# Optimization experiments

Measured on AMD Instinct MI355X. Metric: run time of the kernel, lower is better.

Reference implementation:

```python
import jax, jax.numpy as jnp
import numpy as np

D_MODEL = 1024
N_HEADS = 16
D_K = D_MODEL // N_HEADS
B, T = 2, 2048
EPS = 1e-6


def _phi(x):
    # elu(x) + 1
    return jax.nn.elu(x) + 1.0


def setup_inputs() -> dict:
    key = jax.random.key(0)
    ks = jax.random.split(key, 5)
    s = 1.0 / np.sqrt(D_MODEL)
    return {
        "x": jax.random.normal(ks[0], (B, T, D_MODEL), jnp.float32),
        "Wq": jax.random.normal(ks[1], (D_MODEL, D_MODEL), jnp.float32) * s,
        "bq": jnp.zeros((D_MODEL,), jnp.float32),
        "Wk": jax.random.normal(ks[2], (D_MODEL, D_MODEL), jnp.float32) * s,
        "bk": jnp.zeros((D_MODEL,), jnp.float32),
        "Wv": jax.random.normal(ks[3], (D_MODEL, D_MODEL), jnp.float32) * s,
        "bv": jnp.zeros((D_MODEL,), jnp.float32),
        "Wo": jax.random.normal(ks[4], (D_MODEL, D_MODEL), jnp.float32) * s,
        "bo": jnp.zeros((D_MODEL,), jnp.float32),
    }


def reference(x, Wq, bq, Wk, bk, Wv, bv, Wo, bo):
    Bv_, Tv_, _ = x.shape
    # projections (torch nn.Linear: x @ W.T + b), split heads -> [B, H, T, d_k]
    def proj(W, b):
        y = x @ W.T + b
        return y.reshape(Bv_, Tv_, N_HEADS, D_K).transpose(0, 2, 1, 3)

    q = _phi(proj(Wq, bq))
    k = _phi(proj(Wk, bk))
    v = proj(Wv, bv)

    # causal linear attention: running kv outer-product and k prefix sums
    kv = jnp.einsum("bhtd,bhte->bhtde", k, v)          # [B,H,T,d_k,d_k]
    kv = jnp.cumsum(kv, axis=2)
    k_cum = jnp.cumsum(k, axis=2)
    out = jnp.einsum("bhtd,bhtde->bhte", q, kv)        # [B,H,T,d_k]
    z = jnp.einsum("bhtd,bhtd->bht", q, k_cum)         # [B,H,T]
    out = out / (z[..., None] + EPS)

    out = out.transpose(0, 2, 1, 3).reshape(Bv_, Tv_, N_HEADS * D_K)
    return out @ Wo.T + bo
```

## Files before the change

### kernel.cpp

```cpp
#include <hip/hip_runtime.h>


typedef float  f32x4   __attribute__((ext_vector_type(4)));
typedef __bf16 bf16x8  __attribute__((ext_vector_type(8)));
typedef short  short8v __attribute__((ext_vector_type(8)));
typedef short  short4v __attribute__((ext_vector_type(4)));

static __device__ __forceinline__ short f2bf(float f) {
    unsigned u = __float_as_uint(f);
    u += 0x7FFFu + ((u >> 16) & 1u);
    return (short)(u >> 16);
}
static __device__ __forceinline__ float bf2f(short s) {
    return __uint_as_float(((unsigned)(unsigned short)s) << 16);
}
static __device__ __forceinline__ float phi(float x) {
    return x > 0.f ? x + 1.f : __expf(x);
}
static __device__ __forceinline__ void gl_lds16(const short* g, short* l) {
    __builtin_amdgcn_global_load_lds(
        (const __attribute__((address_space(1))) void*)g,
        (__attribute__((address_space(3))) void*)l, 16, 0, 0);
}

#define LDT 72
static __device__ __forceinline__ int swz(int row, int col) {
    return row * LDT + (col ^ (row & 56));
}

__global__ __launch_bounds__(256) void convert_bf16(
    const float* __restrict__ x,  const float* __restrict__ Wq,
    const float* __restrict__ Wk, const float* __restrict__ Wv,
    const float* __restrict__ Wo,
    short* __restrict__ xb,  short* __restrict__ Wqb,
    short* __restrict__ Wkb, short* __restrict__ Wvb, short* __restrict__ Wob)
{
    const int blk = blockIdx.x;
    const float* src; short* dst; size_t base;
    if (blk < 2048)      { src = x;  dst = xb;  base = (size_t)blk * 2048; }
    else if (blk < 2560) { src = Wq; dst = Wqb; base = (size_t)(blk - 2048) * 2048; }
    else if (blk < 3072) { src = Wk; dst = Wkb; base = (size_t)(blk - 2560) * 2048; }
    else if (blk < 3584) { src = Wv; dst = Wvb; base = (size_t)(blk - 3072) * 2048; }
    else                 { src = Wo; dst = Wob; base = (size_t)(blk - 3584) * 2048; }
    const size_t o = base + (size_t)threadIdx.x * 8;
    f32x4 v0 = *(const f32x4*)&src[o];
    f32x4 v1 = *(const f32x4*)&src[o + 4];
    short8v s;
#pragma unroll
    for (int m = 0; m < 4; ++m) { s[m] = f2bf(v0[m]); s[m + 4] = f2bf(v1[m]); }
    *(short8v*)&dst[o] = s;
}

__global__ __launch_bounds__(256) void gemm_qkv(
    const short* __restrict__ xb,
    const short* __restrict__ Wqb, const short* __restrict__ Wkb,
    const short* __restrict__ Wvb,
    const float* __restrict__ bq, const float* __restrict__ bk,
    const float* __restrict__ bv,
    short* __restrict__ Qb, short* __restrict__ Kb, short* __restrict__ Vb)
{
    __shared__ short As[128 * 32];
    __shared__ short Bs[128 * 32];
    const int tid = threadIdx.x;
    const int bm = blockIdx.x, bn = blockIdx.y;
    const int wsel = bn >> 3;
    const int n0 = (bn & 7) << 7;
    const short* __restrict__ W    = (wsel == 0) ? Wqb : (wsel == 1) ? Wkb : Wvb;
    const float* __restrict__ bias = (wsel == 0) ? bq  : (wsel == 1) ? bk  : bv;
    short* __restrict__ Ob         = (wsel == 0) ? Qb  : (wsel == 1) ? Kb  : Vb;
    const int m0 = bm << 7;
    const int wave = tid >> 6, lane = tid & 63;
    const int wm = (wave & 1) << 6, wn = (wave >> 1) << 6;
    const int l15 = lane & 15, quad = lane >> 4;

    const int ch0 = wave * 2, ch1 = ch0 + 1;
    const int lrow = lane >> 2, lcol = (lane & 3) << 3;
    const short* ga0 = xb + (size_t)(m0 + ch0 * 16 + lrow) * 1024 + lcol;
    const short* ga1 = xb + (size_t)(m0 + ch1 * 16 + lrow) * 1024 + lcol;
    const short* gb0 = W  + (size_t)(n0 + ch0 * 16 + lrow) * 1024 + lcol;
    const short* gb1 = W  + (size_t)(n0 + ch1 * 16 + lrow) * 1024 + lcol;
    short* la0 = &As[ch0 * 512];
    short* la1 = &As[ch1 * 512];
    short* lb0 = &Bs[ch0 * 512];
    short* lb1 = &Bs[ch1 * 512];

    f32x4 acc[4][4] = {};
    for (int k0 = 0; k0 < 1024; k0 += 32) {
        __syncthreads();
        gl_lds16(ga0 + k0, la0);
        gl_lds16(ga1 + k0, la1);
        gl_lds16(gb0 + k0, lb0);
        gl_lds16(gb1 + k0, lb1);
        __syncthreads();
        bf16x8 a[4], b[4];
#pragma unroll
        for (int i = 0; i < 4; ++i) a[i] = *(const bf16x8*)&As[(wm + i * 16 + l15) * 32 + quad * 8];
#pragma unroll
        for (int j = 0; j < 4; ++j) b[j] = *(const bf16x8*)&Bs[(wn + j * 16 + l15) * 32 + quad * 8];
#pragma unroll
        for (int i = 0; i < 4; ++i)
#pragma unroll
            for (int j = 0; j < 4; ++j)
                acc[i][j] = __builtin_amdgcn_mfma_f32_16x16x32_bf16(a[i], b[j], acc[i][j], 0, 0, 0);
    }

#pragma unroll
    for (int i = 0; i < 4; ++i)
#pragma unroll
        for (int j = 0; j < 4; ++j) {
            const int col = n0 + wn + j * 16 + l15;
            const int h = col >> 6, d = col & 63;
            const float bv_ = bias[col];
            const int row0 = m0 + wm + i * 16 + quad * 4;
            const int b = row0 >> 11, t0 = row0 & 2047;
            const size_t obase = ((size_t)(b * 16 + h) * 2048 + t0) * 64 + d;
#pragma unroll
            for (int r = 0; r < 4; ++r) {
                float v = acc[i][j][r] + bv_;
                if (wsel < 2) v = phi(v);
                Ob[obase + (size_t)r * 64] = f2bf(v);
            }
        }
}

__global__ __launch_bounds__(256) void chunk_sums(
    const short* __restrict__ Kb, const short* __restrict__ Vb,
    short* __restrict__ KVsum, float* __restrict__ ksum)
{
    __shared__ short KT[64 * LDT];
    __shared__ short VT[64 * LDT];
    __shared__ float pS[256];
    const int c = blockIdx.x, bh = blockIdx.y;
    const int tid = threadIdx.x;
    const int w = tid >> 6, lane = tid & 63, l15 = lane & 15, quad = lane >> 4;
    const size_t tilebase = ((size_t)bh * 2048 + c * 64) * 64;

    {
        const int t0 = (tid >> 4) << 2;
        const int e0 = (tid & 15) << 2;
        short4v kr[4], vr[4];
#pragma unroll
        for (int i = 0; i < 4; ++i) {
            const size_t g = tilebase + (size_t)(t0 + i) * 64 + e0;
            kr[i] = *(const short4v*)&Kb[g];
            vr[i] = *(const short4v*)&Vb[g];
        }
#pragma unroll
        for (int i = 0; i < 4; ++i) {
            short4v kt, vt;
#pragma unroll
            for (int j = 0; j < 4; ++j) { kt[j] = kr[j][i]; vt[j] = vr[j][i]; }
            *(short4v*)&KT[swz(e0 + i, t0)] = kt;
            *(short4v*)&VT[swz(e0 + i, t0)] = vt;
        }
    }
    __syncthreads();

    f32x4 acc[4] = {};
    __builtin_amdgcn_s_setprio(1);
#pragma unroll
    for (int k0 = 0; k0 < 64; k0 += 32) {
        const int ra = w * 16 + l15;
        bf16x8 a = *(const bf16x8*)&KT[ra * LDT + ((k0 + quad * 8) ^ (ra & 56))];
#pragma unroll
        for (int tj = 0; tj < 4; ++tj) {
            const int rb = tj * 16 + l15;
            bf16x8 bfr = *(const bf16x8*)&VT[rb * LDT + ((k0 + quad * 8) ^ (rb & 56))];
            acc[tj] = __builtin_amdgcn_mfma_f32_16x16x32_bf16(a, bfr, acc[tj], 0, 0, 0);
        }
    }
    __builtin_amdgcn_s_setprio(0);
    short* __restrict__ outp = KVsum + (((size_t)bh * 32) + c) * 4096;
#pragma unroll
    for (int tj = 0; tj < 4; ++tj)
#pragma unroll
        for (int r = 0; r < 4; ++r)
            outp[(w * 16 + quad * 4 + r) * 64 + tj * 16 + l15] = f2bf(acc[tj][r]);

    {
        const int d = tid & 63, part = tid >> 6;
        short8v k1 = *(const short8v*)&KT[d * LDT + ((part * 16) ^ (d & 56))];
        short8v k2 = *(const short8v*)&KT[d * LDT + ((part * 16 + 8) ^ (d & 56))];
        float s = 0.f;
#pragma unroll
        for (int m = 0; m < 8; ++m) s += bf2f(k1[m]) + bf2f(k2[m]);
        pS[part * 64 + d] = s;
    }
    __syncthreads();
    if (tid < 64)
        ksum[(((size_t)bh * 32) + c) * 64 + tid] =
            pS[tid] + pS[tid + 64] + pS[tid + 128] + pS[tid + 192];
}

__global__ __launch_bounds__(256) void scan_chunks(
    const short* __restrict__ KVsum, const float* __restrict__ ksum,
    short* __restrict__ KVpref, float* __restrict__ kpref)
{
    const int bh = blockIdx.y;
    const int o = blockIdx.x * 256 + threadIdx.x;
    float run = 0.f;
    size_t base = (size_t)bh * 32 * 4096 + o;
    for (int cc = 0; cc < 32; ++cc) {
        KVpref[base] = f2bf(run);
        run += bf2f(KVsum[base]);
        base += 4096;
    }
    if (blockIdx.x == 0 && threadIdx.x < 64) {
        float vals[32];
        const size_t kb = (size_t)bh * 32 * 64 + threadIdx.x;
#pragma unroll
        for (int cc = 0; cc < 32; ++cc) vals[cc] = ksum[kb + (size_t)cc * 64];
        float r2 = 0.f;
#pragma unroll
        for (int cc = 0; cc < 32; ++cc) { kpref[kb + (size_t)cc * 64] = r2; r2 += vals[cc]; }
    }
}

__global__ __launch_bounds__(256) void attn_chunk(
    const short* __restrict__ Qb, const short* __restrict__ Kb,
    const short* __restrict__ Vb, const short* __restrict__ KVpref,
    const float* __restrict__ kpref, short* __restrict__ attnb)
{
    __shared__ short Qs[64 * LDT];
    __shared__ short KS[64 * LDT];
    __shared__ short VT[64 * LDT];
    __shared__ short KVT[64 * LDT];
    const int c = blockIdx.x, bh = blockIdx.y;
    const int b = bh >> 4, h = bh & 15;
    const int tid = threadIdx.x;
    const int w = tid >> 6, lane = tid & 63, l15 = lane & 15, quad = lane >> 4;
    const size_t tilebase = ((size_t)bh * 2048 + c * 64) * 64;
    const short* __restrict__ KVc = KVpref + (((size_t)bh * 32) + c) * 4096;

#pragma unroll
    for (int p = 0; p < 2; ++p) {
        const int t = (tid >> 3) + p * 32;
        const int e0q = (tid & 7) << 3;
        const size_t g = tilebase + (size_t)t * 64 + e0q;
        *(short8v*)&Qs[t * LDT + e0q] = *(const short8v*)&Qb[g];
        *(short8v*)&KS[t * LDT + e0q] = *(const short8v*)&Kb[g];
    }
    {
        const int t0 = (tid >> 4) << 2;
        const int e0 = (tid & 15) << 2;
        short4v vr[4], pr[4];
#pragma unroll
        for (int i = 0; i < 4; ++i) {
            const size_t g = tilebase + (size_t)(t0 + i) * 64 + e0;
            vr[i] = *(const short4v*)&Vb[g];
            pr[i] = *(const short4v*)&KVc[(t0 + i) * 64 + e0];
        }
#pragma unroll
        for (int i = 0; i < 4; ++i) {
            short4v vt, pt;
#pragma unroll
            for (int j = 0; j < 4; ++j) { vt[j] = vr[j][i]; pt[j] = pr[j][i]; }
            *(short4v*)&VT[swz(e0 + i, t0)]  = vt;
            *(short4v*)&KVT[swz(e0 + i, t0)] = pt;
        }
    }
    __syncthreads();

    f32x4 sacc[4] = {};
    __builtin_amdgcn_s_setprio(1);
#pragma unroll
    for (int k0 = 0; k0 < 64; k0 += 32) {
        bf16x8 a = *(const bf16x8*)&Qs[(w * 16 + l15) * LDT + k0 + quad * 8];
#pragma unroll
        for (int tj = 0; tj < 4; ++tj) {
            bf16x8 bfr = *(const bf16x8*)&KS[(tj * 16 + l15) * LDT + k0 + quad * 8];
            sacc[tj] = __builtin_amdgcn_mfma_f32_16x16x32_bf16(a, bfr, sacc[tj], 0, 0, 0);
        }
    }
    __builtin_amdgcn_s_setprio(0);

    f32x4 kp4 = *(const f32x4*)&kpref[(((size_t)bh * 32) + c) * 64 + l15 * 4];
    float zinv[4];
#pragma unroll
    for (int r = 0; r < 4; ++r) {
        const int i = w * 16 + quad * 4 + r;
        float p = 0.f;
#pragma unroll
        for (int tj = 0; tj < 4; ++tj)
            if (tj * 16 + l15 <= i) p += sacc[tj][r];
        short4v q4 = *(const short4v*)&Qs[i * LDT + l15 * 4];
#pragma unroll
        for (int m = 0; m < 4; ++m) p += bf2f(q4[m]) * kp4[m];
        p += __shfl_xor(p, 1);
        p += __shfl_xor(p, 2);
        p += __shfl_xor(p, 4);
        p += __shfl_xor(p, 8);
        zinv[r] = 1.f / (p + 1e-6f);
    }

    __syncthreads();
#pragma unroll
    for (int tj = 0; tj < 4; ++tj)
#pragma unroll
        for (int r = 0; r < 4; ++r) {
            const int i = w * 16 + quad * 4 + r;
            const int j = tj * 16 + l15;
            KS[i * LDT + j] = f2bf(j <= i ? sacc[tj][r] : 0.f);
        }

    f32x4 oacc[4] = {};
    __builtin_amdgcn_s_setprio(1);
#pragma unroll
    for (int k0 = 0; k0 < 64; k0 += 32) {
        bf16x8 a1 = *(const bf16x8*)&KS[(w * 16 + l15) * LDT + k0 + quad * 8];
        bf16x8 a2 = *(const bf16x8*)&Qs[(w * 16 + l15) * LDT + k0 + quad * 8];
#pragma unroll
        for (int tj = 0; tj < 4; ++tj) {
            const int rb = tj * 16 + l15;
            bf16x8 b1 = *(const bf16x8*)&VT[rb * LDT + ((k0 + quad * 8) ^ (rb & 56))];
            bf16x8 b2 = *(const bf16x8*)&KVT[rb * LDT + ((k0 + quad * 8) ^ (rb & 56))];
            oacc[tj] = __builtin_amdgcn_mfma_f32_16x16x32_bf16(a1, b1, oacc[tj], 0, 0, 0);
            oacc[tj] = __builtin_amdgcn_mfma_f32_16x16x32_bf16(a2, b2, oacc[tj], 0, 0, 0);
        }
    }
    __builtin_amdgcn_s_setprio(0);
    const size_t arowbase = (size_t)b * 2048 + c * 64;
#pragma unroll
    for (int tj = 0; tj < 4; ++tj)
#pragma unroll
        for (int r = 0; r < 4; ++r) {
            const int i = w * 16 + quad * 4 + r;
            const int e = tj * 16 + l15;
            attnb[(arowbase + i) * 1024 + h * 64 + e] = f2bf(oacc[tj][r] * zinv[r]);
        }
}

__global__ __launch_bounds__(256) void gemm_out(
    const short* __restrict__ attnb, const short* __restrict__ Wob,
    const float* __restrict__ bo, float* __restrict__ outp)
{
    __shared__ short As[128 * 32];
    __shared__ short Bs[64 * 32];
    const int tid = threadIdx.x;
    const int bm = blockIdx.x, bn = blockIdx.y;
    const int m0 = bm << 7, n0 = bn << 6;
    const int wave = tid >> 6, lane = tid & 63;
    const int wm = (wave & 1) << 6, wn = (wave >> 1) << 5;
    const int l15 = lane & 15, quad = lane >> 4;

    const int lrow = lane >> 2, lcol = (lane & 3) << 3;
    const short* gp[3]; short* lp[3];
#pragma unroll
    for (int cc = 0; cc < 3; ++cc) {
        const int ch = wave * 3 + cc;
        if (ch < 8) {
            gp[cc] = attnb + (size_t)(m0 + ch * 16 + lrow) * 1024 + lcol;
            lp[cc] = &As[ch * 512];
        } else {
            gp[cc] = Wob + (size_t)(n0 + (ch - 8) * 16 + lrow) * 1024 + lcol;
            lp[cc] = &Bs[(ch - 8) * 512];
        }
    }

    f32x4 acc[4][2] = {};
    for (int k0 = 0; k0 < 1024; k0 += 32) {
        __syncthreads();
        gl_lds16(gp[0] + k0, lp[0]);
        gl_lds16(gp[1] + k0, lp[1]);
        gl_lds16(gp[2] + k0, lp[2]);
        __syncthreads();
        bf16x8 a[4], b[2];
#pragma unroll
        for (int i = 0; i < 4; ++i) a[i] = *(const bf16x8*)&As[(wm + i * 16 + l15) * 32 + quad * 8];
#pragma unroll
        for (int j = 0; j < 2; ++j) b[j] = *(const bf16x8*)&Bs[(wn + j * 16 + l15) * 32 + quad * 8];
#pragma unroll
        for (int i = 0; i < 4; ++i)
#pragma unroll
            for (int j = 0; j < 2; ++j)
                acc[i][j] = __builtin_amdgcn_mfma_f32_16x16x32_bf16(a[i], b[j], acc[i][j], 0, 0, 0);
    }

#pragma unroll
    for (int i = 0; i < 4; ++i)
#pragma unroll
        for (int j = 0; j < 2; ++j) {
            const int col = n0 + wn + j * 16 + l15;
            const float bv_ = bo[col];
#pragma unroll
            for (int r = 0; r < 4; ++r) {
                const int row = m0 + wm + i * 16 + quad * 4 + r;
                outp[(size_t)row * 1024 + col] = acc[i][j][r] + bv_;
            }
        }
}

extern "C" void kernel_launch(void* const* d_in, const int* in_sizes, int n_in,
                              void* d_out, int out_size, void* d_ws, size_t ws_size,
                              hipStream_t stream)
{
    const float* x  = (const float*)d_in[0];
    const float* Wq = (const float*)d_in[1];
    const float* bq = (const float*)d_in[2];
    const float* Wk = (const float*)d_in[3];
    const float* bk = (const float*)d_in[4];
    const float* Wv = (const float*)d_in[5];
    const float* bv = (const float*)d_in[6];
    const float* Wo = (const float*)d_in[7];
    const float* bo = (const float*)d_in[8];

    char* ws = (char*)d_ws;
    short* xb     = (short*)(ws + 0);
    short* Wqb    = (short*)(ws + 8388608);
    short* Wkb    = (short*)(ws + 10485760);
    short* Wvb    = (short*)(ws + 12582912);
    short* Wob    = (short*)(ws + 14680064);
    short* Qb     = (short*)(ws + 16777216);
    short* Kb     = (short*)(ws + 25165824);
    short* Vb     = (short*)(ws + 33554432);
    short* KVsum  = (short*)(ws + 41943040);
    short* KVpref = (short*)(ws + 50331648);
    short* attnb  = (short*)(ws + 58720256);
    float* ksum   = (float*)(ws + 67108864);
    float* kpref  = (float*)(ws + 67371008);
    float* outp   = (float*)d_out;

    convert_bf16<<<4096, 256, 0, stream>>>(x, Wq, Wk, Wv, Wo, xb, Wqb, Wkb, Wvb, Wob);
    gemm_qkv   <<<dim3(32, 24), 256, 0, stream>>>(xb, Wqb, Wkb, Wvb, bq, bk, bv, Qb, Kb, Vb);
    chunk_sums <<<dim3(32, 32), 256, 0, stream>>>(Kb, Vb, KVsum, ksum);
    scan_chunks<<<dim3(16, 32), 256, 0, stream>>>(KVsum, ksum, KVpref, kpref);
    attn_chunk <<<dim3(32, 32), 256, 0, stream>>>(Qb, Kb, Vb, KVpref, kpref, attnb);
    gemm_out   <<<dim3(32, 16), 256, 0, stream>>>(attnb, Wob, bo, outp);
}
```

Measured before the change: 161.6 us.

## Fuse chunk prefix scan into attention kernel, dropping scan_chunks launch

Removes the separate scan_chunks kernel. Each attn_chunk block now sums the KV chunk sums and k sums of all earlier chunks itself to build its prefix state. This saves one launch and the KVpref/kpref write and read round trip. In exchange, the work becomes redundant: block c reads c earlier 8KB tiles, giving O(C^2) total reads and an imbalanced load that grows with chunk index.

```diff
diff --git a/kernel.cpp b/kernel.cpp
--- a/kernel.cpp
+++ b/kernel.cpp
@@ -192,34 +192,10 @@
             pS[tid] + pS[tid + 64] + pS[tid + 128] + pS[tid + 192];
 }
 
-__global__ __launch_bounds__(256) void scan_chunks(
-    const short* __restrict__ KVsum, const float* __restrict__ ksum,
-    short* __restrict__ KVpref, float* __restrict__ kpref)
-{
-    const int bh = blockIdx.y;
-    const int o = blockIdx.x * 256 + threadIdx.x;
-    float run = 0.f;
-    size_t base = (size_t)bh * 32 * 4096 + o;
-    for (int cc = 0; cc < 32; ++cc) {
-        KVpref[base] = f2bf(run);
-        run += bf2f(KVsum[base]);
-        base += 4096;
-    }
-    if (blockIdx.x == 0 && threadIdx.x < 64) {
-        float vals[32];
-        const size_t kb = (size_t)bh * 32 * 64 + threadIdx.x;
-#pragma unroll
-        for (int cc = 0; cc < 32; ++cc) vals[cc] = ksum[kb + (size_t)cc * 64];
-        float r2 = 0.f;
-#pragma unroll
-        for (int cc = 0; cc < 32; ++cc) { kpref[kb + (size_t)cc * 64] = r2; r2 += vals[cc]; }
-    }
-}
-
 __global__ __launch_bounds__(256) void attn_chunk(
     const short* __restrict__ Qb, const short* __restrict__ Kb,
-    const short* __restrict__ Vb, const short* __restrict__ KVpref,
-    const float* __restrict__ kpref, short* __restrict__ attnb)
+    const short* __restrict__ Vb, const short* __restrict__ KVsum,
+    const float* __restrict__ ksum, short* __restrict__ attnb)
 {
     __shared__ short Qs[64 * LDT];
     __shared__ short KS[64 * LDT];
@@ -230,7 +206,7 @@
     const int tid = threadIdx.x;
     const int w = tid >> 6, lane = tid & 63, l15 = lane & 15, quad = lane >> 4;
     const size_t tilebase = ((size_t)bh * 2048 + c * 64) * 64;
-    const short* __restrict__ KVc = KVpref + (((size_t)bh * 32) + c) * 4096;
+    const short* __restrict__ KVbase = KVsum + ((size_t)bh * 32) * 4096;
 
 #pragma unroll
     for (int p = 0; p < 2; ++p) {
@@ -240,23 +216,45 @@
         *(short8v*)&Qs[t * LDT + e0q] = *(const short8v*)&Qb[g];
         *(short8v*)&KS[t * LDT + e0q] = *(const short8v*)&Kb[g];
     }
+    const int t0 = (tid >> 4) << 2;
+    const int e0 = (tid & 15) << 2;
     {
-        const int t0 = (tid >> 4) << 2;
-        const int e0 = (tid & 15) << 2;
-        short4v vr[4], pr[4];
+        short4v vr[4];
+#pragma unroll
+        for (int i = 0; i < 4; ++i)
+            vr[i] = *(const short4v*)&Vb[tilebase + (size_t)(t0 + i) * 64 + e0];
 #pragma unroll
         for (int i = 0; i < 4; ++i) {
-            const size_t g = tilebase + (size_t)(t0 + i) * 64 + e0;
-            vr[i] = *(const short4v*)&Vb[g];
-            pr[i] = *(const short4v*)&KVc[(t0 + i) * 64 + e0];
-        }
+            short4v vt;
+#pragma unroll
+            for (int j = 0; j < 4; ++j) vt[j] = vr[j][i];
+            *(short4v*)&VT[swz(e0 + i, t0)] = vt;
+        }
+    }
+    float pacc[4][4] = {};
+    for (int cc = 0; cc < c; ++cc) {
+        const short* tp = KVbase + (size_t)cc * 4096;
 #pragma unroll
         for (int i = 0; i < 4; ++i) {
-            short4v vt, pt;
-#pragma unroll
-            for (int j = 0; j < 4; ++j) { vt[j] = vr[j][i]; pt[j] = pr[j][i]; }
-            *(short4v*)&VT[swz(e0 + i, t0)]  = vt;
-            *(short4v*)&KVT[swz(e0 + i, t0)] = pt;
+            short4v s = *(const short4v*)&tp[(t0 + i) * 64 + e0];
+#pragma unroll
+            for (int j = 0; j < 4; ++j) pacc[i][j] += bf2f(s[j]);
+        }
+    }
+#pragma unroll
+    for (int j = 0; j < 4; ++j) {
+        short4v pt;
+#pragma unroll
+        for (int i = 0; i < 4; ++i) pt[i] = f2bf(pacc[i][j]);
+        *(short4v*)&KVT[swz(e0 + j, t0)] = pt;
+    }
+    f32x4 kp4 = {0.f, 0.f, 0.f, 0.f};
+    {
+        const float* kb_ = ksum + ((size_t)bh * 32) * 64 + l15 * 4;
+        for (int cc = 0; cc < c; ++cc) {
+            f32x4 kv = *(const f32x4*)&kb_[(size_t)cc * 64];
+#pragma unroll
+            for (int m = 0; m < 4; ++m) kp4[m] += kv[m];
         }
     }
     __syncthreads();
@@ -274,7 +272,6 @@
     }
     __builtin_amdgcn_s_setprio(0);
 
-    f32x4 kp4 = *(const f32x4*)&kpref[(((size_t)bh * 32) + c) * 64 + l15 * 4];
     float zinv[4];
 #pragma unroll
     for (int r = 0; r < 4; ++r) {
@@ -414,16 +411,13 @@
     short* Kb     = (short*)(ws + 25165824);
     short* Vb     = (short*)(ws + 33554432);
     short* KVsum  = (short*)(ws + 41943040);
-    short* KVpref = (short*)(ws + 50331648);
-    short* attnb  = (short*)(ws + 58720256);
-    float* ksum   = (float*)(ws + 67108864);
-    float* kpref  = (float*)(ws + 67371008);
+    short* attnb  = (short*)(ws + 50331648);
+    float* ksum   = (float*)(ws + 58720256);
     float* outp   = (float*)d_out;
 
     convert_bf16<<<4096, 256, 0, stream>>>(x, Wq, Wk, Wv, Wo, xb, Wqb, Wkb, Wvb, Wob);
     gemm_qkv   <<<dim3(32, 24), 256, 0, stream>>>(xb, Wqb, Wkb, Wvb, bq, bk, bv, Qb, Kb, Vb);
     chunk_sums <<<dim3(32, 32), 256, 0, stream>>>(Kb, Vb, KVsum, ksum);
-    scan_chunks<<<dim3(16, 32), 256, 0, stream>>>(KVsum, ksum, KVpref, kpref);
-    attn_chunk <<<dim3(32, 32), 256, 0, stream>>>(Qb, Kb, Vb, KVpref, kpref, attnb);
+    attn_chunk <<<dim3(32, 32), 256, 0, stream>>>(Qb, Kb, Vb, KVsum, ksum, attnb);
     gemm_out   <<<dim3(32, 16), 256, 0, stream>>>(attnb, Wob, bo, outp);
 }
```

Result: slower. 172.9 us (+7.1%).
